# Kernel optimization log

Measured on AMD Instinct MI355X. Metric: run time of the kernel, lower is better.

The kernel has to match this reference:

```python
import jax, jax.numpy as jnp
import numpy as np

BS, L, D = 32, 512, 512
N_CHARS = 32
DICT = 97

def setup_inputs() -> dict:
    key = jax.random.key(0)
    ks = jax.random.split(key, 10)
    s = 1.0 / np.sqrt(D)
    return {
        "inp": jax.random.normal(ks[0], (BS, L, D), jnp.float32),
        "emb": jax.random.normal(ks[1], (N_CHARS, D), jnp.float32) * 0.02,  # embedding table; char_orders == arange
        "Wo_w": jax.random.normal(ks[2], (D, D), jnp.float32) * s,
        "Wo_b": jnp.zeros((D,), jnp.float32),
        "Wv_w": jax.random.normal(ks[3], (D, D), jnp.float32) * s,
        "Wv_b": jnp.zeros((D,), jnp.float32),
        "We_w": jax.random.normal(ks[4], (D, 1), jnp.float32) * s,
        "We_b": jnp.zeros((1,), jnp.float32),
        "Wc_w": jax.random.normal(ks[5], (D, DICT), jnp.float32) * s,
        "Wc_b": jnp.zeros((DICT,), jnp.float32),
    }

def reference(inp, emb, Wo_w, Wo_b, Wv_w, Wv_b, We_w, We_b, Wc_w, Wc_b):
    # O = embedding(arange(max_n_chars)) is just the full embedding table: (n, d)
    w_o = emb @ Wo_w + Wo_b                      # (n, d)
    w_v = inp @ Wv_w + Wv_b                      # (b, L, d)
    # broadcast add -> tanh -> score projection: (b, n, L, d) -> (b, n, L)
    h = jnp.tanh(w_o[None, :, None, :] + w_v[:, None, :, :])
    e = jnp.einsum('bnld,d->bnl', h, We_w[:, 0]) + We_b[0]
    alpha = jax.nn.softmax(e, axis=2)            # softmax over L (axis=2)
    visual_features = jnp.einsum('bnl,bld->bnd', alpha, inp)  # (b, n, d)
    logits = visual_features @ Wc_w + Wc_b       # (b, n, dict)
    return (visual_features, logits)
```

## Files before the change

kernel.cpp:

```cpp
#include <hip/hip_runtime.h>
#include <hip/hip_bf16.h>

#define BS    32
#define LSEQ  512
#define DIM   512
#define NCH   32
#define NDICT 97
#define CHB   16

#define TANH_SCALE 2.8853900817779268f

typedef __attribute__((ext_vector_type(8))) short bf16x8;
typedef __attribute__((ext_vector_type(4))) float f32x4;

#define GLDS16(gsrc, ldst) \
  __builtin_amdgcn_global_load_lds((const __attribute__((address_space(1))) void*)(gsrc), \
                                   (__attribute__((address_space(3))) void*)(ldst), 16, 0, 0)

__device__ __forceinline__ float sig_from_scaled(float xs) {
    float e2 = __builtin_amdgcn_exp2f(xs);
    return __builtin_amdgcn_rcpf(1.0f + e2);
}

__device__ __forceinline__ void split_bf16(float a, ushort& h, ushort& l) {
    __hip_bfloat16 bh = __float2bfloat16(a);
    float fh = __bfloat162float(bh);
    __hip_bfloat16 bl = __float2bfloat16(a - fh);
    h = *(ushort*)&bh; l = *(ushort*)&bl;
}

__global__ __launch_bounds__(256) void k_misc(
    const float* __restrict__ Wv, ushort* __restrict__ BhiT, ushort* __restrict__ BloT,
    const float* __restrict__ emb, const float* __restrict__ Wo_w,
    const float* __restrict__ Wo_b, float* __restrict__ w_o)
{
    __shared__ float tile[64][65];
    const int bid = blockIdx.x;
    const int t = threadIdx.x;
    if (bid < 64) {
        const int k0 = (bid >> 3) * 64, n0 = (bid & 7) * 64;
        const int tr = t >> 4, tc = (t & 15) * 4;
        #pragma unroll
        for (int rr = 0; rr < 64; rr += 16) {
            float4 v = *(const float4*)&Wv[(k0 + rr + tr) * DIM + n0 + tc];
            tile[rr + tr][tc + 0] = v.x; tile[rr + tr][tc + 1] = v.y;
            tile[rr + tr][tc + 2] = v.z; tile[rr + tr][tc + 3] = v.w;
        }
        __syncthreads();
        #pragma unroll
        for (int rr = 0; rr < 64; rr += 16) {
            const int n = rr + tr;
            ushort4 h, l;
            split_bf16(tile[tc + 0][n] * TANH_SCALE, h.x, l.x);
            split_bf16(tile[tc + 1][n] * TANH_SCALE, h.y, l.y);
            split_bf16(tile[tc + 2][n] * TANH_SCALE, h.z, l.z);
            split_bf16(tile[tc + 3][n] * TANH_SCALE, h.w, l.w);
            *(ushort4*)&BhiT[(size_t)(n0 + n) * DIM + k0 + tc] = h;
            *(ushort4*)&BloT[(size_t)(n0 + n) * DIM + k0 + tc] = l;
        }
    } else {
        const int n = bid - 64;
        float* embS = &tile[0][0];
        embS[t]       = emb[n * DIM + t];
        embS[t + 256] = emb[n * DIM + t + 256];
        __syncthreads();
        float acc0 = Wo_b[t], acc1 = Wo_b[t + 256];
        for (int k = 0; k < DIM; ++k) {
            float ek = embS[k];
            acc0 = fmaf(ek, Wo_w[k * DIM + t], acc0);
            acc1 = fmaf(ek, Wo_w[k * DIM + t + 256], acc1);
        }
        w_o[n * DIM + t]       = acc0 * TANH_SCALE;
        w_o[n * DIM + t + 256] = acc1 * TANH_SCALE;
    }
}

__global__ __launch_bounds__(256) void k_gemm(
    const float* __restrict__ A,
    const ushort* __restrict__ Bhi, const ushort* __restrict__ Blo,
    const float* __restrict__ bias, float* __restrict__ C)
{
    __shared__ ushort Bh[128 * 64], Bl[128 * 64];

    const int bid = blockIdx.x;
    const int mb = (bid & 7) * 16 + (bid >> 5);
    const int nb = (bid >> 3) & 3;
    const int bm = mb * 128, bn = nb * 128;

    const int t = threadIdx.x;
    const int wave = t >> 6, lane = t & 63;
    const int wm = wave >> 1, wn = wave & 1;

    const int rl = lane >> 3;
    const int gsw = (lane & 7) ^ rl;

    const int am = bm + wm * 64 + (lane & 15);
    const int ak = (lane >> 4) * 8;

    f32x4 acc[4][4] = {};

    for (int k0 = 0; k0 < DIM; k0 += 64) {
        bf16x8 ah[4][2], al[4][2];
        #pragma unroll
        for (int i = 0; i < 4; ++i)
            #pragma unroll
            for (int kh = 0; kh < 2; ++kh) {
                const float* ap = A + (size_t)(am + i * 16) * DIM + k0 + kh * 32 + ak;
                float4 v0 = *(const float4*)ap;
                float4 v1 = *(const float4*)(ap + 4);
                float vv[8] = {v0.x, v0.y, v0.z, v0.w, v1.x, v1.y, v1.z, v1.w};
                bf16x8 h, l;
                #pragma unroll
                for (int q = 0; q < 8; ++q) {
                    ushort hq, lq; split_bf16(vv[q], hq, lq);
                    h[q] = (short)hq; l[q] = (short)lq;
                }
                ah[i][kh] = h; al[i][kh] = l;
            }
        #pragma unroll
        for (int c4 = 0; c4 < 4; ++c4) {
            const int c = wave * 4 + c4;
            const size_t rb = (size_t)(bn + c * 8 + rl) * DIM + k0 + gsw * 8;
            GLDS16(Bhi + rb, &Bh[c * 512]);
            GLDS16(Blo + rb, &Bl[c * 512]);
        }
        __syncthreads();

        #pragma unroll
        for (int kh = 0; kh < 2; ++kh) {
            const int p = ((kh * 4 + (lane >> 4)) ^ (lane & 7)) * 8;
            bf16x8 bh[4], bl[4];
            #pragma unroll
            for (int j = 0; j < 4; ++j) {
                const int rbr = (wn * 64 + j * 16 + (lane & 15)) * 64 + p;
                bh[j] = *(const bf16x8*)&Bh[rbr];
                bl[j] = *(const bf16x8*)&Bl[rbr];
            }
            #pragma unroll
            for (int i = 0; i < 4; ++i)
                #pragma unroll
                for (int j = 0; j < 4; ++j) {
                    acc[i][j] = __builtin_amdgcn_mfma_f32_16x16x32_bf16(ah[i][kh], bh[j], acc[i][j], 0, 0, 0);
                    acc[i][j] = __builtin_amdgcn_mfma_f32_16x16x32_bf16(ah[i][kh], bl[j], acc[i][j], 0, 0, 0);
                    acc[i][j] = __builtin_amdgcn_mfma_f32_16x16x32_bf16(al[i][kh], bh[j], acc[i][j], 0, 0, 0);
                }
        }
        __syncthreads();
    }

    #pragma unroll
    for (int i = 0; i < 4; ++i) {
        const int m = bm + wm * 64 + i * 16 + (lane >> 4) * 4;
        #pragma unroll
        for (int j = 0; j < 4; ++j) {
            const int n = bn + wn * 64 + j * 16 + (lane & 15);
            const float bb = TANH_SCALE * bias[n];
            #pragma unroll
            for (int r = 0; r < 4; ++r)
                C[(size_t)(m + r) * DIM + n] = acc[i][j][r] + bb;
        }
    }
}

__global__ __launch_bounds__(256, 4) void k_e(
    const float* __restrict__ w_v, const float* __restrict__ w_o,
    const float* __restrict__ We_w, float* __restrict__ e)
{
    __shared__ float4 woS[CHB * 128];
    const int lblk = blockIdx.x;
    const int b    = blockIdx.y;
    const int ch0  = blockIdx.z * CHB;
    const int t    = threadIdx.x;

    const float4* wog = ((const float4*)w_o) + ch0 * (DIM / 4);
    #pragma unroll
    for (int i = 0; i < 8; ++i)
        woS[t + 256 * i] = wog[t + 256 * i];

    const int wave = t >> 6, lane = t & 63;
    const int g = lane >> 4, j = lane & 15;
    const int l = lblk * 16 + wave * 4 + g;

    const float4* wvp = (const float4*)(w_v + (size_t)(b * LSEQ + l) * DIM);
    const float4* wep = (const float4*)We_w;
    float4 wv[8], we[8];
    #pragma unroll
    for (int k = 0; k < 8; ++k) {
        wv[k] = wvp[16 * k + j];
        we[k] = wep[16 * k + j];
    }
    float wsum = 0.0f;
    #pragma unroll
    for (int k = 0; k < 8; ++k)
        wsum += (we[k].x + we[k].y) + (we[k].z + we[k].w);
    #pragma unroll
    for (int off = 1; off < 16; off <<= 1) wsum += __shfl_xor(wsum, off, 64);

    __syncthreads();

    float res = 0.0f;
    for (int i = 0; i < CHB; ++i) {
        const float4* wrow = &woS[i * 128];
        float s = 0.0f;
        #pragma unroll
        for (int k = 0; k < 8; ++k) {
            float4 wo4 = wrow[16 * k + j];
            s = fmaf(we[k].x, sig_from_scaled(wo4.x + wv[k].x), s);
            s = fmaf(we[k].y, sig_from_scaled(wo4.y + wv[k].y), s);
            s = fmaf(we[k].z, sig_from_scaled(wo4.z + wv[k].z), s);
            s = fmaf(we[k].w, sig_from_scaled(wo4.w + wv[k].w), s);
        }
        #pragma unroll
        for (int off = 1; off < 16; off <<= 1) s += __shfl_xor(s, off, 64);
        if (j == i) res = s;
    }
    e[(size_t)(b * NCH + ch0 + j) * LSEQ + l] = fmaf(-2.0f, res, wsum);
}

__global__ __launch_bounds__(256) void k_soft(
    const float* __restrict__ e, ushort* __restrict__ aH, ushort* __restrict__ aL)
{
    const int row = blockIdx.x * 4 + (threadIdx.x >> 6);
    const int lane = threadIdx.x & 63;
    const float4* erow = (const float4*)(e + (size_t)row * LSEQ);
    float4 v0 = erow[2 * lane], v1 = erow[2 * lane + 1];
    float m = fmaxf(fmaxf(fmaxf(v0.x, v0.y), fmaxf(v0.z, v0.w)),
                    fmaxf(fmaxf(v1.x, v1.y), fmaxf(v1.z, v1.w)));
    #pragma unroll
    for (int off = 32; off > 0; off >>= 1) m = fmaxf(m, __shfl_xor(m, off, 64));
    float p[8];
    p[0] = __expf(v0.x - m); p[1] = __expf(v0.y - m);
    p[2] = __expf(v0.z - m); p[3] = __expf(v0.w - m);
    p[4] = __expf(v1.x - m); p[5] = __expf(v1.y - m);
    p[6] = __expf(v1.z - m); p[7] = __expf(v1.w - m);
    float s = ((p[0] + p[1]) + (p[2] + p[3])) + ((p[4] + p[5]) + (p[6] + p[7]));
    #pragma unroll
    for (int off = 32; off > 0; off >>= 1) s += __shfl_xor(s, off, 64);
    const float inv = 1.0f / s;
    ushort4 h0, h1, l0, l1;
    split_bf16(p[0] * inv, h0.x, l0.x); split_bf16(p[1] * inv, h0.y, l0.y);
    split_bf16(p[2] * inv, h0.z, l0.z); split_bf16(p[3] * inv, h0.w, l0.w);
    split_bf16(p[4] * inv, h1.x, l1.x); split_bf16(p[5] * inv, h1.y, l1.y);
    split_bf16(p[6] * inv, h1.z, l1.z); split_bf16(p[7] * inv, h1.w, l1.w);
    ushort4* oh = (ushort4*)(aH + (size_t)row * LSEQ);
    ushort4* ol = (ushort4*)(aL + (size_t)row * LSEQ);
    oh[2 * lane] = h0; oh[2 * lane + 1] = h1;
    ol[2 * lane] = l0; ol[2 * lane + 1] = l1;
}

__global__ __launch_bounds__(256) void k_vf(
    const float* __restrict__ inp,
    const ushort* __restrict__ aH, const ushort* __restrict__ aL,
    float* __restrict__ out_vf)
{
    __shared__ unsigned int tT[64 * 68];
    const int dg = blockIdx.x, b = blockIdx.y;
    const int t = threadIdx.x;
    const int wave = t >> 6, lane = t & 63;
    const int d0 = dg * 64;
    const int lr = t >> 2;
    const int dcb = (t & 3) * 4;

    const ushort* aHb = aH + (size_t)b * NCH * LSEQ + (size_t)(lane & 15) * LSEQ;
    const ushort* aLb = aL + (size_t)b * NCH * LSEQ + (size_t)(lane & 15) * LSEQ;
    const int dl = wave * 16 + (lane & 15);
    const int lloc = (lane >> 4) * 8;

    f32x4 acc[2] = {};

    for (int l0 = 0; l0 < LSEQ; l0 += 64) {
        #pragma unroll
        for (int q = 0; q < 4; ++q) {
            const int dc = dcb + 16 * q;
            float4 v = *(const float4*)&inp[((size_t)(b * LSEQ) + l0 + lr) * DIM + d0 + dc];
            float vv[4] = {v.x, v.y, v.z, v.w};
            #pragma unroll
            for (int i = 0; i < 4; ++i) {
                ushort h, l; split_bf16(vv[i], h, l);
                const int d = dc + i;
                const int g = (lr >> 3) ^ (d & 7);
                tT[d * 68 + g * 8 + (lr & 7)] = ((unsigned)l << 16) | (unsigned)h;
            }
        }
        __syncthreads();
        #pragma unroll
        for (int sl = 0; sl < 2; ++sl) {
            const int ll = sl * 32 + lloc;
            const int gg = ((ll >> 3) ^ (dl & 7)) * 8;
            const uint4* srcp = (const uint4*)&tT[dl * 68 + gg];
            uint4 w0 = srcp[0], w1 = srcp[1];
            union { unsigned u[4]; bf16x8 v; } H, L;
            H.u[0] = (w0.x & 0xFFFFu) | (w0.y << 16);
            H.u[1] = (w0.z & 0xFFFFu) | (w0.w << 16);
            H.u[2] = (w1.x & 0xFFFFu) | (w1.y << 16);
            H.u[3] = (w1.z & 0xFFFFu) | (w1.w << 16);
            L.u[0] = (w0.x >> 16) | (w0.y & 0xFFFF0000u);
            L.u[1] = (w0.z >> 16) | (w0.w & 0xFFFF0000u);
            L.u[2] = (w1.x >> 16) | (w1.y & 0xFFFF0000u);
            L.u[3] = (w1.z >> 16) | (w1.w & 0xFFFF0000u);

            const bf16x8 ah0 = *(const bf16x8*)&aHb[l0 + ll];
            const bf16x8 ah1 = *(const bf16x8*)&aHb[16 * LSEQ + l0 + ll];
            const bf16x8 al0 = *(const bf16x8*)&aLb[l0 + ll];
            const bf16x8 al1 = *(const bf16x8*)&aLb[16 * LSEQ + l0 + ll];

            acc[0] = __builtin_amdgcn_mfma_f32_16x16x32_bf16(ah0, H.v, acc[0], 0, 0, 0);
            acc[0] = __builtin_amdgcn_mfma_f32_16x16x32_bf16(ah0, L.v, acc[0], 0, 0, 0);
            acc[0] = __builtin_amdgcn_mfma_f32_16x16x32_bf16(al0, H.v, acc[0], 0, 0, 0);
            acc[1] = __builtin_amdgcn_mfma_f32_16x16x32_bf16(ah1, H.v, acc[1], 0, 0, 0);
            acc[1] = __builtin_amdgcn_mfma_f32_16x16x32_bf16(ah1, L.v, acc[1], 0, 0, 0);
            acc[1] = __builtin_amdgcn_mfma_f32_16x16x32_bf16(al1, H.v, acc[1], 0, 0, 0);
        }
        __syncthreads();
    }

    const int dcol = d0 + dl;
    #pragma unroll
    for (int m = 0; m < 2; ++m) {
        const int ch = m * 16 + (lane >> 4) * 4;
        #pragma unroll
        for (int r = 0; r < 4; ++r)
            out_vf[(size_t)(b * NCH + ch + r) * DIM + dcol] = acc[m][r];
    }
}

__global__ __launch_bounds__(256) void k_lg(
    const float* __restrict__ vf, const float* __restrict__ Wc_w,
    const float* __restrict__ Wc_b, float* __restrict__ out_logits)
{
    __shared__ float vfS[4][DIM];
    __shared__ float lgS[2][4][NDICT];
    const int r0 = blockIdx.x * 4;
    const int t = threadIdx.x;
    const int wave = t >> 6, lane = t & 63;

    const float2* src = (const float2*)(vf + (size_t)(r0 + wave) * DIM);
    #pragma unroll
    for (int q = 0; q < 4; ++q)
        ((float2*)&vfS[wave][0])[lane + 64 * q] = src[lane + 64 * q];
    __syncthreads();

    const int j = t & 127, half = t >> 7;
    if (j < NDICT) {
        const float* wc = Wc_w + (size_t)half * 256 * NDICT + j;
        const float* v0 = &vfS[0][half * 256];
        const float* v1 = &vfS[1][half * 256];
        const float* v2 = &vfS[2][half * 256];
        const float* v3 = &vfS[3][half * 256];
        float a0 = 0.f, a1 = 0.f, a2 = 0.f, a3 = 0.f;
        #pragma unroll 4
        for (int d = 0; d < 256; ++d) {
            float w = wc[(size_t)d * NDICT];
            a0 = fmaf(v0[d], w, a0); a1 = fmaf(v1[d], w, a1);
            a2 = fmaf(v2[d], w, a2); a3 = fmaf(v3[d], w, a3);
        }
        lgS[half][0][j] = a0; lgS[half][1][j] = a1;
        lgS[half][2][j] = a2; lgS[half][3][j] = a3;
    }
    __syncthreads();
    for (int idx = t; idx < 4 * NDICT; idx += 256) {
        const int r = idx / NDICT, jj = idx - r * NDICT;
        out_logits[(size_t)(r0 + r) * NDICT + jj] = Wc_b[jj] + lgS[0][r][jj] + lgS[1][r][jj];
    }
}

extern "C" void kernel_launch(void* const* d_in, const int* in_sizes, int n_in,
                              void* d_out, int out_size, void* d_ws, size_t ws_size,
                              hipStream_t stream)
{
    const float* inp  = (const float*)d_in[0];
    const float* emb  = (const float*)d_in[1];
    const float* Wo_w = (const float*)d_in[2];
    const float* Wo_b = (const float*)d_in[3];
    const float* Wv_w = (const float*)d_in[4];
    const float* Wv_b = (const float*)d_in[5];
    const float* We_w = (const float*)d_in[6];
    const float* Wc_w = (const float*)d_in[8];
    const float* Wc_b = (const float*)d_in[9];

    char* p = (char*)d_ws;
    float*  w_o  = (float*)p;   p += (64 << 10);
    float*  ev   = (float*)p;   p += (size_t)BS * NCH * LSEQ * 4;
    ushort* BhiT = (ushort*)p;  p += (size_t)DIM * DIM * 2;
    ushort* BloT = (ushort*)p;  p += (size_t)DIM * DIM * 2;
    ushort* aH   = (ushort*)p;  p += (size_t)BS * NCH * LSEQ * 2;
    ushort* aL   = (ushort*)p;  p += (size_t)BS * NCH * LSEQ * 2;
    float*  w_v  = (float*)p;

    float* out_vf = (float*)d_out;
    float* out_lg = out_vf + BS * NCH * DIM;

    k_misc<<<dim3(96), dim3(256), 0, stream>>>(Wv_w, BhiT, BloT, emb, Wo_w, Wo_b, w_o);
    k_gemm<<<dim3(512), dim3(256), 0, stream>>>(inp, BhiT, BloT, Wv_b, w_v);
    k_e<<<dim3(LSEQ / 16, BS, NCH / CHB), dim3(256), 0, stream>>>(w_v, w_o, We_w, ev);
    k_soft<<<dim3(256), dim3(256), 0, stream>>>(ev, aH, aL);
    k_vf<<<dim3(8, BS), dim3(256), 0, stream>>>(inp, aH, aL, out_vf);
    k_lg<<<dim3(256), dim3(256), 0, stream>>>(out_vf, Wc_w, Wc_b, out_lg);
}
```

Before: 170.8 us.

## Move emb@Wo onto MFMA blocks in GEMM, cheapen bf16 split, shrink k_e channel block

The scalar emb@Wo_w product in k_misc becomes extra MFMA blocks appended to the w_v GEMM launch, working on split-bf16 copies of Wo and emb that k_misc now prepares. The split into high and low bf16 parts is replaced by integer bit tricks that handle pairs. k_e drops from 16 to 8 channels per block with higher occupancy bounds and four independent accumulators. The scalar w_o loop was a slow serial tail, and removing it is the main intent. Costs are extra workspace and an added transpose pass over Wo. The new split rounds the high part differently, but the hi+lo sum should still be exact.

```diff
diff --git a/kernel.cpp b/kernel.cpp
--- a/kernel.cpp
+++ b/kernel.cpp
@@ -6,7 +6,7 @@
 #define DIM   512
 #define NCH   32
 #define NDICT 97
-#define CHB   16
+#define CHB   8
 
 #define TANH_SCALE 2.8853900817779268f
 
@@ -22,27 +22,36 @@
     return __builtin_amdgcn_rcpf(1.0f + e2);
 }
 
-__device__ __forceinline__ void split_bf16(float a, ushort& h, ushort& l) {
-    __hip_bfloat16 bh = __float2bfloat16(a);
-    float fh = __bfloat162float(bh);
-    __hip_bfloat16 bl = __float2bfloat16(a - fh);
-    h = *(ushort*)&bh; l = *(ushort*)&bl;
+__device__ __forceinline__ void split2u(float x0, float x1, unsigned& hp, unsigned& lp) {
+    unsigned r0 = __float_as_uint(x0) + 0x8000u;
+    unsigned r1 = __float_as_uint(x1) + 0x8000u;
+    float f0 = __uint_as_float(r0 & 0xFFFF0000u);
+    float f1 = __uint_as_float(r1 & 0xFFFF0000u);
+    hp = (r0 >> 16) | (r1 & 0xFFFF0000u);
+    unsigned s0 = __float_as_uint(x0 - f0);
+    unsigned s1 = __float_as_uint(x1 - f1);
+    lp = (s0 >> 16) | (s1 & 0xFFFF0000u);
 }
 
 __global__ __launch_bounds__(256) void k_misc(
     const float* __restrict__ Wv, ushort* __restrict__ BhiT, ushort* __restrict__ BloT,
-    const float* __restrict__ emb, const float* __restrict__ Wo_w,
-    const float* __restrict__ Wo_b, float* __restrict__ w_o)
+    const float* __restrict__ Wo, ushort* __restrict__ WohiT, ushort* __restrict__ WoloT,
+    const float* __restrict__ emb, ushort* __restrict__ embH, ushort* __restrict__ embL)
 {
     __shared__ float tile[64][65];
     const int bid = blockIdx.x;
     const int t = threadIdx.x;
-    if (bid < 64) {
-        const int k0 = (bid >> 3) * 64, n0 = (bid & 7) * 64;
+    if (bid < 128) {
+        const bool isWv = bid < 64;
+        const float* src = isWv ? Wv : Wo;
+        ushort* dH = isWv ? BhiT : WohiT;
+        ushort* dL = isWv ? BloT : WoloT;
+        const int bb = bid & 63;
+        const int k0 = (bb >> 3) * 64, n0 = (bb & 7) * 64;
         const int tr = t >> 4, tc = (t & 15) * 4;
         #pragma unroll
         for (int rr = 0; rr < 64; rr += 16) {
-            float4 v = *(const float4*)&Wv[(k0 + rr + tr) * DIM + n0 + tc];
+            float4 v = *(const float4*)&src[(size_t)(k0 + rr + tr) * DIM + n0 + tc];
             tile[rr + tr][tc + 0] = v.x; tile[rr + tr][tc + 1] = v.y;
             tile[rr + tr][tc + 2] = v.z; tile[rr + tr][tc + 3] = v.w;
         }
@@ -50,119 +59,170 @@
         #pragma unroll
         for (int rr = 0; rr < 64; rr += 16) {
             const int n = rr + tr;
-            ushort4 h, l;
-            split_bf16(tile[tc + 0][n] * TANH_SCALE, h.x, l.x);
-            split_bf16(tile[tc + 1][n] * TANH_SCALE, h.y, l.y);
-            split_bf16(tile[tc + 2][n] * TANH_SCALE, h.z, l.z);
-            split_bf16(tile[tc + 3][n] * TANH_SCALE, h.w, l.w);
-            *(ushort4*)&BhiT[(size_t)(n0 + n) * DIM + k0 + tc] = h;
-            *(ushort4*)&BloT[(size_t)(n0 + n) * DIM + k0 + tc] = l;
+            unsigned h01, l01, h23, l23;
+            split2u(tile[tc + 0][n] * TANH_SCALE, tile[tc + 1][n] * TANH_SCALE, h01, l01);
+            split2u(tile[tc + 2][n] * TANH_SCALE, tile[tc + 3][n] * TANH_SCALE, h23, l23);
+            *(uint2*)&dH[(size_t)(n0 + n) * DIM + k0 + tc] = make_uint2(h01, h23);
+            *(uint2*)&dL[(size_t)(n0 + n) * DIM + k0 + tc] = make_uint2(l01, l23);
         }
     } else {
-        const int n = bid - 64;
-        float* embS = &tile[0][0];
-        embS[t]       = emb[n * DIM + t];
-        embS[t + 256] = emb[n * DIM + t + 256];
-        __syncthreads();
-        float acc0 = Wo_b[t], acc1 = Wo_b[t + 256];
-        for (int k = 0; k < DIM; ++k) {
-            float ek = embS[k];
-            acc0 = fmaf(ek, Wo_w[k * DIM + t], acc0);
-            acc1 = fmaf(ek, Wo_w[k * DIM + t + 256], acc1);
-        }
-        w_o[n * DIM + t]       = acc0 * TANH_SCALE;
-        w_o[n * DIM + t + 256] = acc1 * TANH_SCALE;
+        for (int i = t; i < 4096; i += 256) {
+            float4 v = ((const float4*)emb)[i];
+            unsigned h01, l01, h23, l23;
+            split2u(v.x, v.y, h01, l01);
+            split2u(v.z, v.w, h23, l23);
+            ((uint2*)embH)[i] = make_uint2(h01, h23);
+            ((uint2*)embL)[i] = make_uint2(l01, l23);
+        }
     }
 }
 
 __global__ __launch_bounds__(256) void k_gemm(
     const float* __restrict__ A,
     const ushort* __restrict__ Bhi, const ushort* __restrict__ Blo,
-    const float* __restrict__ bias, float* __restrict__ C)
+    const float* __restrict__ bias, float* __restrict__ C,
+    const ushort* __restrict__ WohiT, const ushort* __restrict__ WoloT,
+    const ushort* __restrict__ embH, const ushort* __restrict__ embL,
+    const float* __restrict__ Wo_b, float* __restrict__ w_o)
 {
     __shared__ ushort Bh[128 * 64], Bl[128 * 64];
 
     const int bid = blockIdx.x;
-    const int mb = (bid & 7) * 16 + (bid >> 5);
-    const int nb = (bid >> 3) & 3;
-    const int bm = mb * 128, bn = nb * 128;
-
     const int t = threadIdx.x;
     const int wave = t >> 6, lane = t & 63;
-    const int wm = wave >> 1, wn = wave & 1;
-
     const int rl = lane >> 3;
     const int gsw = (lane & 7) ^ rl;
 
-    const int am = bm + wm * 64 + (lane & 15);
-    const int ak = (lane >> 4) * 8;
-
-    f32x4 acc[4][4] = {};
-
-    for (int k0 = 0; k0 < DIM; k0 += 64) {
-        bf16x8 ah[4][2], al[4][2];
-        #pragma unroll
-        for (int i = 0; i < 4; ++i)
+    if (bid < 512) {
+        const int mb = (bid & 7) * 16 + (bid >> 5);
+        const int nb = (bid >> 3) & 3;
+        const int bm = mb * 128, bn = nb * 128;
+        const int wm = wave >> 1, wn = wave & 1;
+        const int am = bm + wm * 64 + (lane & 15);
+        const int ak = (lane >> 4) * 8;
+
+        f32x4 acc[4][4] = {};
+
+        for (int k0 = 0; k0 < DIM; k0 += 64) {
+            bf16x8 ah[4][2], al[4][2];
+            #pragma unroll
+            for (int i = 0; i < 4; ++i)
+                #pragma unroll
+                for (int kh = 0; kh < 2; ++kh) {
+                    const float* ap = A + (size_t)(am + i * 16) * DIM + k0 + kh * 32 + ak;
+                    float4 v0 = *(const float4*)ap;
+                    float4 v1 = *(const float4*)(ap + 4);
+                    union { unsigned u[4]; bf16x8 v; } H, L;
+                    split2u(v0.x, v0.y, H.u[0], L.u[0]);
+                    split2u(v0.z, v0.w, H.u[1], L.u[1]);
+                    split2u(v1.x, v1.y, H.u[2], L.u[2]);
+                    split2u(v1.z, v1.w, H.u[3], L.u[3]);
+                    ah[i][kh] = H.v; al[i][kh] = L.v;
+                }
+            #pragma unroll
+            for (int c4 = 0; c4 < 4; ++c4) {
+                const int c = wave * 4 + c4;
+                const size_t rb = (size_t)(bn + c * 8 + rl) * DIM + k0 + gsw * 8;
+                GLDS16(Bhi + rb, &Bh[c * 512]);
+                GLDS16(Blo + rb, &Bl[c * 512]);
+            }
+            __syncthreads();
+
             #pragma unroll
             for (int kh = 0; kh < 2; ++kh) {
-                const float* ap = A + (size_t)(am + i * 16) * DIM + k0 + kh * 32 + ak;
-                float4 v0 = *(const float4*)ap;
-                float4 v1 = *(const float4*)(ap + 4);
-                float vv[8] = {v0.x, v0.y, v0.z, v0.w, v1.x, v1.y, v1.z, v1.w};
-                bf16x8 h, l;
-                #pragma unroll
-                for (int q = 0; q < 8; ++q) {
-                    ushort hq, lq; split_bf16(vv[q], hq, lq);
-                    h[q] = (short)hq; l[q] = (short)lq;
+                const int p = ((kh * 4 + (lane >> 4)) ^ (lane & 7)) * 8;
+                bf16x8 bh[4], bl[4];
+                #pragma unroll
+                for (int j = 0; j < 4; ++j) {
+                    const int rbr = (wn * 64 + j * 16 + (lane & 15)) * 64 + p;
+                    bh[j] = *(const bf16x8*)&Bh[rbr];
+                    bl[j] = *(const bf16x8*)&Bl[rbr];
                 }
-                ah[i][kh] = h; al[i][kh] = l;
-            }
-        #pragma unroll
-        for (int c4 = 0; c4 < 4; ++c4) {
-            const int c = wave * 4 + c4;
-            const size_t rb = (size_t)(bn + c * 8 + rl) * DIM + k0 + gsw * 8;
-            GLDS16(Bhi + rb, &Bh[c * 512]);
-            GLDS16(Blo + rb, &Bl[c * 512]);
-        }
-        __syncthreads();
-
-        #pragma unroll
-        for (int kh = 0; kh < 2; ++kh) {
-            const int p = ((kh * 4 + (lane >> 4)) ^ (lane & 7)) * 8;
-            bf16x8 bh[4], bl[4];
+                #pragma unroll
+                for (int i = 0; i < 4; ++i)
+                    #pragma unroll
+                    for (int j = 0; j < 4; ++j) {
+                        acc[i][j] = __builtin_amdgcn_mfma_f32_16x16x32_bf16(ah[i][kh], bh[j], acc[i][j], 0, 0, 0);
+                        acc[i][j] = __builtin_amdgcn_mfma_f32_16x16x32_bf16(ah[i][kh], bl[j], acc[i][j], 0, 0, 0);
+                        acc[i][j] = __builtin_amdgcn_mfma_f32_16x16x32_bf16(al[i][kh], bh[j], acc[i][j], 0, 0, 0);
+                    }
+            }
+            __syncthreads();
+        }
+
+        #pragma unroll
+        for (int i = 0; i < 4; ++i) {
+            const int m = bm + wm * 64 + i * 16 + (lane >> 4) * 4;
             #pragma unroll
             for (int j = 0; j < 4; ++j) {
-                const int rbr = (wn * 64 + j * 16 + (lane & 15)) * 64 + p;
-                bh[j] = *(const bf16x8*)&Bh[rbr];
-                bl[j] = *(const bf16x8*)&Bl[rbr];
-            }
-            #pragma unroll
-            for (int i = 0; i < 4; ++i)
-                #pragma unroll
-                for (int j = 0; j < 4; ++j) {
-                    acc[i][j] = __builtin_amdgcn_mfma_f32_16x16x32_bf16(ah[i][kh], bh[j], acc[i][j], 0, 0, 0);
-                    acc[i][j] = __builtin_amdgcn_mfma_f32_16x16x32_bf16(ah[i][kh], bl[j], acc[i][j], 0, 0, 0);
-                    acc[i][j] = __builtin_amdgcn_mfma_f32_16x16x32_bf16(al[i][kh], bh[j], acc[i][j], 0, 0, 0);
+                const int n = bn + wn * 64 + j * 16 + (lane & 15);
+                const float bb = TANH_SCALE * bias[n];
+                #pragma unroll
+                for (int r = 0; r < 4; ++r)
+                    C[(size_t)(m + r) * DIM + n] = acc[i][j][r] + bb;
+            }
+        }
+    } else {
+        const int nb0 = (bid - 512) * 128;
+        f32x4 acc[2][2] = {};
+
+        for (int k0 = 0; k0 < DIM; k0 += 64) {
+            bf16x8 eh[2][2], el[2][2];
+            #pragma unroll
+            for (int m = 0; m < 2; ++m)
+                #pragma unroll
+                for (int kh = 0; kh < 2; ++kh) {
+                    const size_t ra = (size_t)(m * 16 + (lane & 15)) * DIM + k0 + kh * 32 + (lane >> 4) * 8;
+                    eh[m][kh] = *(const bf16x8*)&embH[ra];
+                    el[m][kh] = *(const bf16x8*)&embL[ra];
                 }
-        }
-        __syncthreads();
-    }
-
-    #pragma unroll
-    for (int i = 0; i < 4; ++i) {
-        const int m = bm + wm * 64 + i * 16 + (lane >> 4) * 4;
-        #pragma unroll
-        for (int j = 0; j < 4; ++j) {
-            const int n = bn + wn * 64 + j * 16 + (lane & 15);
-            const float bb = TANH_SCALE * bias[n];
-            #pragma unroll
-            for (int r = 0; r < 4; ++r)
-                C[(size_t)(m + r) * DIM + n] = acc[i][j][r] + bb;
-        }
-    }
-}
-
-__global__ __launch_bounds__(256, 4) void k_e(
+            #pragma unroll
+            for (int c4 = 0; c4 < 4; ++c4) {
+                const int c = wave * 4 + c4;
+                const size_t rb = (size_t)(nb0 + c * 8 + rl) * DIM + k0 + gsw * 8;
+                GLDS16(WohiT + rb, &Bh[c * 512]);
+                GLDS16(WoloT + rb, &Bl[c * 512]);
+            }
+            __syncthreads();
+
+            #pragma unroll
+            for (int kh = 0; kh < 2; ++kh) {
+                const int p = ((kh * 4 + (lane >> 4)) ^ (lane & 7)) * 8;
+                bf16x8 bh[2], bl[2];
+                #pragma unroll
+                for (int j = 0; j < 2; ++j) {
+                    const int rbr = (wave * 32 + j * 16 + (lane & 15)) * 64 + p;
+                    bh[j] = *(const bf16x8*)&Bh[rbr];
+                    bl[j] = *(const bf16x8*)&Bl[rbr];
+                }
+                #pragma unroll
+                for (int m = 0; m < 2; ++m)
+                    #pragma unroll
+                    for (int j = 0; j < 2; ++j) {
+                        acc[m][j] = __builtin_amdgcn_mfma_f32_16x16x32_bf16(eh[m][kh], bh[j], acc[m][j], 0, 0, 0);
+                        acc[m][j] = __builtin_amdgcn_mfma_f32_16x16x32_bf16(eh[m][kh], bl[j], acc[m][j], 0, 0, 0);
+                        acc[m][j] = __builtin_amdgcn_mfma_f32_16x16x32_bf16(el[m][kh], bh[j], acc[m][j], 0, 0, 0);
+                    }
+            }
+            __syncthreads();
+        }
+
+        #pragma unroll
+        for (int m = 0; m < 2; ++m) {
+            const int row = m * 16 + (lane >> 4) * 4;
+            #pragma unroll
+            for (int j = 0; j < 2; ++j) {
+                const int col = nb0 + wave * 32 + j * 16 + (lane & 15);
+                const float bb = TANH_SCALE * Wo_b[col];
+                #pragma unroll
+                for (int r = 0; r < 4; ++r)
+                    w_o[(size_t)(row + r) * DIM + col] = acc[m][j][r] + bb;
+            }
+        }
+    }
+}
+
+__global__ __launch_bounds__(256, 8) void k_e(
     const float* __restrict__ w_v, const float* __restrict__ w_o,
     const float* __restrict__ We_w, float* __restrict__ e)
 {
@@ -174,7 +234,7 @@
 
     const float4* wog = ((const float4*)w_o) + ch0 * (DIM / 4);
     #pragma unroll
-    for (int i = 0; i < 8; ++i)
+    for (int i = 0; i < CHB * 128 / 256; ++i)
         woS[t + 256 * i] = wog[t + 256 * i];
 
     const int wave = t >> 6, lane = t & 63;
@@ -201,20 +261,22 @@
     float res = 0.0f;
     for (int i = 0; i < CHB; ++i) {
         const float4* wrow = &woS[i * 128];
-        float s = 0.0f;
+        float s0 = 0.f, s1 = 0.f, s2 = 0.f, s3 = 0.f;
         #pragma unroll
         for (int k = 0; k < 8; ++k) {
             float4 wo4 = wrow[16 * k + j];
-            s = fmaf(we[k].x, sig_from_scaled(wo4.x + wv[k].x), s);
-            s = fmaf(we[k].y, sig_from_scaled(wo4.y + wv[k].y), s);
-            s = fmaf(we[k].z, sig_from_scaled(wo4.z + wv[k].z), s);
-            s = fmaf(we[k].w, sig_from_scaled(wo4.w + wv[k].w), s);
-        }
+            s0 = fmaf(we[k].x, sig_from_scaled(wo4.x + wv[k].x), s0);
+            s1 = fmaf(we[k].y, sig_from_scaled(wo4.y + wv[k].y), s1);
+            s2 = fmaf(we[k].z, sig_from_scaled(wo4.z + wv[k].z), s2);
+            s3 = fmaf(we[k].w, sig_from_scaled(wo4.w + wv[k].w), s3);
+        }
+        float s = (s0 + s1) + (s2 + s3);
         #pragma unroll
         for (int off = 1; off < 16; off <<= 1) s += __shfl_xor(s, off, 64);
         if (j == i) res = s;
     }
-    e[(size_t)(b * NCH + ch0 + j) * LSEQ + l] = fmaf(-2.0f, res, wsum);
+    if (j < CHB)
+        e[(size_t)(b * NCH + ch0 + j) * LSEQ + l] = fmaf(-2.0f, res, wsum);
 }
 
 __global__ __launch_bounds__(256) void k_soft(
@@ -237,15 +299,17 @@
     #pragma unroll
     for (int off = 32; off > 0; off >>= 1) s += __shfl_xor(s, off, 64);
     const float inv = 1.0f / s;
-    ushort4 h0, h1, l0, l1;
-    split_bf16(p[0] * inv, h0.x, l0.x); split_bf16(p[1] * inv, h0.y, l0.y);
-    split_bf16(p[2] * inv, h0.z, l0.z); split_bf16(p[3] * inv, h0.w, l0.w);
-    split_bf16(p[4] * inv, h1.x, l1.x); split_bf16(p[5] * inv, h1.y, l1.y);
-    split_bf16(p[6] * inv, h1.z, l1.z); split_bf16(p[7] * inv, h1.w, l1.w);
-    ushort4* oh = (ushort4*)(aH + (size_t)row * LSEQ);
-    ushort4* ol = (ushort4*)(aL + (size_t)row * LSEQ);
-    oh[2 * lane] = h0; oh[2 * lane + 1] = h1;
-    ol[2 * lane] = l0; ol[2 * lane + 1] = l1;
+    unsigned h01, l01, h23, l23, h45, l45, h67, l67;
+    split2u(p[0] * inv, p[1] * inv, h01, l01);
+    split2u(p[2] * inv, p[3] * inv, h23, l23);
+    split2u(p[4] * inv, p[5] * inv, h45, l45);
+    split2u(p[6] * inv, p[7] * inv, h67, l67);
+    uint2* oh = (uint2*)(aH + (size_t)row * LSEQ);
+    uint2* ol = (uint2*)(aL + (size_t)row * LSEQ);
+    oh[2 * lane]     = make_uint2(h01, h23);
+    oh[2 * lane + 1] = make_uint2(h45, h67);
+    ol[2 * lane]     = make_uint2(l01, l23);
+    ol[2 * lane + 1] = make_uint2(l45, l67);
 }
 
 __global__ __launch_bounds__(256) void k_vf(
@@ -273,13 +337,19 @@
         for (int q = 0; q < 4; ++q) {
             const int dc = dcb + 16 * q;
             float4 v = *(const float4*)&inp[((size_t)(b * LSEQ) + l0 + lr) * DIM + d0 + dc];
-            float vv[4] = {v.x, v.y, v.z, v.w};
+            unsigned h01, l01, h23, l23;
+            split2u(v.x, v.y, h01, l01);
+            split2u(v.z, v.w, h23, l23);
+            unsigned e0 = (l01 << 16) | (h01 & 0xFFFFu);
+            unsigned e1 = (l01 & 0xFFFF0000u) | (h01 >> 16);
+            unsigned e2 = (l23 << 16) | (h23 & 0xFFFFu);
+            unsigned e3 = (l23 & 0xFFFF0000u) | (h23 >> 16);
+            unsigned ev[4] = {e0, e1, e2, e3};
             #pragma unroll
             for (int i = 0; i < 4; ++i) {
-                ushort h, l; split_bf16(vv[i], h, l);
                 const int d = dc + i;
                 const int g = (lr >> 3) ^ (d & 7);
-                tT[d * 68 + g * 8 + (lr & 7)] = ((unsigned)l << 16) | (unsigned)h;
+                tT[d * 68 + g * 8 + (lr & 7)] = ev[i];
             }
         }
         __syncthreads();
@@ -379,19 +449,24 @@
     const float* Wc_b = (const float*)d_in[9];
 
     char* p = (char*)d_ws;
-    float*  w_o  = (float*)p;   p += (64 << 10);
-    float*  ev   = (float*)p;   p += (size_t)BS * NCH * LSEQ * 4;
-    ushort* BhiT = (ushort*)p;  p += (size_t)DIM * DIM * 2;
-    ushort* BloT = (ushort*)p;  p += (size_t)DIM * DIM * 2;
-    ushort* aH   = (ushort*)p;  p += (size_t)BS * NCH * LSEQ * 2;
-    ushort* aL   = (ushort*)p;  p += (size_t)BS * NCH * LSEQ * 2;
-    float*  w_v  = (float*)p;
+    float*  w_o   = (float*)p;  p += (64 << 10);
+    float*  ev    = (float*)p;  p += (size_t)BS * NCH * LSEQ * 4;
+    ushort* BhiT  = (ushort*)p; p += (size_t)DIM * DIM * 2;
+    ushort* BloT  = (ushort*)p; p += (size_t)DIM * DIM * 2;
+    ushort* WohiT = (ushort*)p; p += (size_t)DIM * DIM * 2;
+    ushort* WoloT = (ushort*)p; p += (size_t)DIM * DIM * 2;
+    ushort* embH  = (ushort*)p; p += (size_t)NCH * DIM * 2;
+    ushort* embL  = (ushort*)p; p += (size_t)NCH * DIM * 2;
+    ushort* aH    = (ushort*)p; p += (size_t)BS * NCH * LSEQ * 2;
+    ushort* aL    = (ushort*)p; p += (size_t)BS * NCH * LSEQ * 2;
+    float*  w_v   = (float*)p;
 
     float* out_vf = (float*)d_out;
     float* out_lg = out_vf + BS * NCH * DIM;
 
-    k_misc<<<dim3(96), dim3(256), 0, stream>>>(Wv_w, BhiT, BloT, emb, Wo_w, Wo_b, w_o);
-    k_gemm<<<dim3(512), dim3(256), 0, stream>>>(inp, BhiT, BloT, Wv_b, w_v);
+    k_misc<<<dim3(129), dim3(256), 0, stream>>>(Wv_w, BhiT, BloT, Wo_w, WohiT, WoloT, emb, embH, embL);
+    k_gemm<<<dim3(516), dim3(256), 0, stream>>>(inp, BhiT, BloT, Wv_b, w_v,
+                                                WohiT, WoloT, embH, embL, Wo_b, w_o);
     k_e<<<dim3(LSEQ / 16, BS, NCH / CHB), dim3(256), 0, stream>>>(w_v, w_o, We_w, ev);
     k_soft<<<dim3(256), dim3(256), 0, stream>>>(ev, aH, aL);
     k_vf<<<dim3(8, BS), dim3(256), 0, stream>>>(inp, aH, aL, out_vf);
```

New measurement: 298.1 us. 74.5% more time.
